# Performance work log

Measured on AMD Instinct MI355X. Metric: run time of the kernel, lower is better.

## Reference

```python
import jax, jax.numpy as jnp
import numpy as np
import math

B, S, D, H, DH, R = 2, 2048, 1024, 16, 64, 8
EPS = 1e-5


def setup_inputs() -> dict:
    key = jax.random.key(0)
    ks = jax.random.split(key, 8)
    hidden_states = jax.random.normal(ks[0], (B, S, D), jnp.float32)
    # causal boolean mask (batch, seq, seq); every row has >=1 valid entry
    causal = jnp.tril(jnp.ones((S, S), dtype=bool))
    attention_mask = jnp.broadcast_to(causal, (B, S, S))
    # lora: (n_layers=1, 4, batch, hidden, rank); [0]=qA,[1]=kA,[2]=qB,[3]=kB
    lora = jax.random.normal(ks[1], (1, 4, B, D, R), jnp.float32) * 0.02
    ln_w = jnp.ones((D,), jnp.float32)
    Wq = jax.random.normal(ks[2], (D, D), jnp.float32) * 0.02
    Wk = jax.random.normal(ks[3], (D, D), jnp.float32) * 0.02
    Wv = jax.random.normal(ks[4], (D, D), jnp.float32) * 0.02
    Wo = jax.random.normal(ks[5], (D, D), jnp.float32) * 0.02
    return dict(hidden_states=hidden_states, attention_mask=attention_mask,
                lora=lora, ln_w=ln_w, Wq=Wq, Wk=Wk, Wv=Wv, Wo=Wo)


def _rms_ln(x, w):
    # model_center LayerNorm with bias=False == RMS layernorm
    var = jnp.mean(x * x, axis=-1, keepdims=True)
    return x * jax.lax.rsqrt(var + EPS) * w


def _lora_delta(h, A, Bm):
    # h: (b,s,D), A: (b,D,R), Bm: (b,R,D);  h + (h@A)@Bm * 2
    z = jnp.einsum('bsd,bdr->bsr', h, A)
    return h + jnp.einsum('bsr,brd->bsd', z, Bm) * 2


def reference(hidden_states, attention_mask, lora, ln_w, Wq, Wk, Wv, Wo):
    b, s, _ = hidden_states.shape
    x = _rms_ln(hidden_states, ln_w)
    h_q = x @ Wq.T
    h_k = x @ Wk.T
    h_v = x @ Wv.T
    layer = lora[0]  # (4, b, D, R)
    h_q = _lora_delta(h_q, layer[0], jnp.swapaxes(layer[2], 1, 2))
    h_k = _lora_delta(h_k, layer[1], jnp.swapaxes(layer[3], 1, 2))
    q = h_q.reshape(b, s, H, DH)
    k = h_k.reshape(b, s, H, DH)
    v = h_v.reshape(b, s, H, DH)
    score = jnp.einsum('bqhd,bkhd->bhqk', q, k) / math.sqrt(DH)
    m = attention_mask[:, None, :, :]  # (b,1,s,s)
    score = jnp.where(m, score, -jnp.inf)
    p = jax.nn.softmax(score, axis=-1)
    p = jnp.where(m, p, jnp.float32(0))
    out = jnp.einsum('bhqk,bkhd->bqhd', p, v).reshape(b, s, H * DH)
    out = out @ Wo.T
    return hidden_states + out
```

## Files before the change

### kernel.cpp

```cpp
#include <hip/hip_runtime.h>

typedef __bf16 bf16;
typedef __bf16 bf16x4 __attribute__((ext_vector_type(4)));
typedef __bf16 bf16x8 __attribute__((ext_vector_type(8)));
typedef float f32x4 __attribute__((ext_vector_type(4)));

#define DM 1024
#define NROW 4096
#define SEQ 2048
#define HDIM 64
#define NEGBIG -30000.0f

#define SWB(base, row, bcol) \
  ((char*)(base) + (row) * 128 + ((bcol) ^ (((row) & 7) << 4)))

__device__ __forceinline__ void async16(const bf16* g, bf16* l) {
  __builtin_amdgcn_global_load_lds(
      (const __attribute__((address_space(1))) unsigned int*)g,
      (__attribute__((address_space(3))) unsigned int*)l, 16, 0, 0);
}

template <bool F32OUT>
__device__ __forceinline__ void gemm128(const bf16* __restrict__ A,
                                        const bf16* __restrict__ Bw,
                                        bf16* __restrict__ Cb,
                                        float* __restrict__ Cf,
                                        const float* __restrict__ resid,
                                        int m0, int n0) {
  __shared__ __align__(16) bf16 sA[128 * 32];
  __shared__ __align__(16) bf16 sB[128 * 32];
  const int t = threadIdx.x;
  const int lane = t & 63;
  const int w = t >> 6;
  const int wm = (w & 1) * 64;
  const int wn = (w >> 1) * 64;
  const int lr = lane & 15;
  const int kg = lane >> 4;

  f32x4 acc[4][4];
#pragma unroll
  for (int i = 0; i < 4; i++)
#pragma unroll
    for (int j = 0; j < 4; j++)
#pragma unroll
      for (int r = 0; r < 4; r++) acc[i][j][r] = 0.0f;

  const int srow = t >> 2;
  const int scol = (t & 3) * 8;
  const bf16* gA = A + (size_t)(m0 + srow) * DM + scol;
  const bf16* gB = Bw + (size_t)(n0 + srow) * DM + scol;
  bf16* lA = &sA[t * 8];
  bf16* lB = &sB[t * 8];

  for (int k0 = 0; k0 < DM; k0 += 32) {
    async16(gA + k0, lA);
    async16(gA + k0 + 64 * DM, lA + 2048);
    async16(gB + k0, lB);
    async16(gB + k0 + 64 * DM, lB + 2048);
    __syncthreads();
    bf16x8 av[4], bv[4];
#pragma unroll
    for (int mi = 0; mi < 4; mi++)
      av[mi] = *(const bf16x8*)&sA[(wm + mi * 16 + lr) * 32 + kg * 8];
#pragma unroll
    for (int nj = 0; nj < 4; nj++)
      bv[nj] = *(const bf16x8*)&sB[(wn + nj * 16 + lr) * 32 + kg * 8];
#pragma unroll
    for (int mi = 0; mi < 4; mi++)
#pragma unroll
      for (int nj = 0; nj < 4; nj++)
        acc[mi][nj] = __builtin_amdgcn_mfma_f32_16x16x32_bf16(av[mi], bv[nj],
                                                              acc[mi][nj], 0, 0, 0);
    __syncthreads();
  }

#pragma unroll
  for (int mi = 0; mi < 4; mi++) {
#pragma unroll
    for (int r = 0; r < 4; r++) {
      const int grow = m0 + wm + mi * 16 + kg * 4 + r;
      const size_t base = (size_t)grow * DM + n0 + wn + lr;
#pragma unroll
      for (int nj = 0; nj < 4; nj++) {
        float v = acc[mi][nj][r];
        if (F32OUT) {
          Cf[base + nj * 16] = v + resid[base + nj * 16];
        } else {
          Cb[base + nj * 16] = (bf16)v;
        }
      }
    }
  }
}

__global__ __launch_bounds__(256) void k_pre(const float* __restrict__ hin,
                                             const float* __restrict__ wln,
                                             const float* __restrict__ Wq,
                                             const float* __restrict__ Wk,
                                             const float* __restrict__ Wv,
                                             const float* __restrict__ Wo,
                                             bf16* __restrict__ xo,
                                             bf16* __restrict__ wcast) {
  __shared__ float red[4];
  const int t = threadIdx.x;
  const int bb = blockIdx.x;
  if (bb < NROW) {
    const int row = bb;
    const float4 h4 = ((const float4*)(hin + (size_t)row * DM))[t];
    float ss = h4.x * h4.x + h4.y * h4.y + h4.z * h4.z + h4.w * h4.w;
#pragma unroll
    for (int off = 1; off < 64; off <<= 1) ss += __shfl_xor(ss, off, 64);
    if ((t & 63) == 0) red[t >> 6] = ss;
    __syncthreads();
    ss = red[0] + red[1] + red[2] + red[3];
    const float inv = rsqrtf(ss * (1.0f / DM) + 1e-5f);
    const float4 w4 = ((const float4*)wln)[t];
    bf16x4 o;
    o[0] = (bf16)(h4.x * inv * w4.x);
    o[1] = (bf16)(h4.y * inv * w4.y);
    o[2] = (bf16)(h4.z * inv * w4.z);
    o[3] = (bf16)(h4.w * inv * w4.w);
    *(bf16x4*)&xo[(size_t)row * DM + t * 4] = o;
  } else {
    const int i = (bb - NROW) * 256 + t;
    const int mat = i >> 18;
    const int off = i & 262143;
    const float* s = (mat == 0) ? Wq : (mat == 1) ? Wk : (mat == 2) ? Wv : Wo;
    const float4 v = ((const float4*)s)[off];
    bf16x4 o;
    o[0] = (bf16)v.x; o[1] = (bf16)v.y; o[2] = (bf16)v.z; o[3] = (bf16)v.w;
    ((bf16x4*)wcast)[i] = o;
  }
}

__global__ __launch_bounds__(256) void k_qkv(const bf16* __restrict__ x,
                                             const bf16* __restrict__ Wq,
                                             const bf16* __restrict__ Wk,
                                             const bf16* __restrict__ Wv,
                                             bf16* __restrict__ hq,
                                             bf16* __restrict__ hk,
                                             bf16* __restrict__ hv) {
  const int nb = blockIdx.y;
  const int wsel = nb >> 3;
  const int n0 = (nb & 7) * 128;
  const bf16* Bw = (wsel == 0) ? Wq : (wsel == 1) ? Wk : Wv;
  bf16* C = (wsel == 0) ? hq : (wsel == 1) ? hk : hv;
  gemm128<false>(x, Bw, C, nullptr, nullptr, blockIdx.x * 128, n0);
}

__global__ __launch_bounds__(256) void k_oproj(const bf16* __restrict__ ctx,
                                               const bf16* __restrict__ Wo,
                                               const float* __restrict__ resid,
                                               float* __restrict__ out) {
  gemm128<true>(ctx, Wo, nullptr, out, resid, blockIdx.x * 128, blockIdx.y * 128);
}

__global__ __launch_bounds__(256) void k_mid(const bf16* __restrict__ hv,
                                             bf16* __restrict__ hvT,
                                             bf16* __restrict__ hq,
                                             bf16* __restrict__ hk,
                                             const float* __restrict__ lora) {
  __shared__ __align__(16) char smem[18432];
  const int t = threadIdx.x;
  const int bb = blockIdx.x;
  const int lane = t & 63;
  const int w = t >> 6;
  const int lr = lane & 15;
  const int kg = lane >> 4;

  if (bb < 1024) {
    bf16* sT = (bf16*)smem;
    const int s0 = (bb & 31) * 64;
    const int c0 = ((bb >> 5) & 15) * 64;
    const int b = bb >> 9;
    const int r = t >> 2;
    const int cc = (t & 3) * 16;
    const bf16* g = hv + ((size_t)(b * SEQ + s0 + r)) * DM + c0 + cc;
    const bf16x8 a0 = *(const bf16x8*)g;
    const bf16x8 a1 = *(const bf16x8*)(g + 8);
    *(bf16x8*)SWB(sT, r, cc * 2) = a0;
    *(bf16x8*)SWB(sT, r, cc * 2 + 16) = a1;
    __syncthreads();
    bf16x8 o0, o1;
#pragma unroll
    for (int j = 0; j < 8; j++) {
      o0[j] = *(const bf16*)SWB(sT, cc + j, r * 2);
      o1[j] = *(const bf16*)SWB(sT, cc + 8 + j, r * 2);
    }
    bf16* o = hvT + ((size_t)(b * DM + c0 + r)) * SEQ + s0 + cc;
    *(bf16x8*)o = o0;
    *(bf16x8*)(o + 8) = o1;
  } else {
    bf16* At = (bf16*)smem;
    float* Zp = (float*)(smem + 16384);
    const int lid = bb - 1024;
    const int row0 = (lid & 127) * 32;
    const int which = lid >> 7;
    const int b = row0 >> 11;
    bf16* H = (which == 0 ? hq : hk) + (size_t)row0 * DM;
    const float* Am = lora + (size_t)(which == 0 ? 0 : 1) * 16384 + (size_t)b * 8192;
    const float* Bm = lora + (size_t)(which == 0 ? 2 : 3) * 16384 + (size_t)b * 8192;

    const int d0 = lane * 16;
    float4 Bv[32];
    {
      const float4* bp = (const float4*)(Bm + (size_t)d0 * 8);
#pragma unroll
      for (int i = 0; i < 32; i++) Bv[i] = bp[i];
    }

    {
      const float4* ap = (const float4*)(Am + (size_t)t * 32);
#pragma unroll
      for (int i = 0; i < 8; i++) {
        const float4 v = ap[i];
        const int idx = t * 32 + i * 4;
        At[(idx & 7) * 1024 + (idx >> 3)]             = (bf16)v.x;
        At[((idx + 1) & 7) * 1024 + ((idx + 1) >> 3)] = (bf16)v.y;
        At[((idx + 2) & 7) * 1024 + ((idx + 2) >> 3)] = (bf16)v.z;
        At[((idx + 3) & 7) * 1024 + ((idx + 3) >> 3)] = (bf16)v.w;
      }
    }
    __syncthreads();

    const int tile = w & 1;
    const int khalf = w >> 1;
    {
      f32x4 zacc;
#pragma unroll
      for (int r = 0; r < 4; r++) zacc[r] = 0.f;
      const bf16* gH = H + (size_t)(tile * 16 + lr) * DM + khalf * 512 + kg * 8;
      const bf16* lA = &At[(lr & 7) * 1024 + khalf * 512 + kg * 8];
#pragma unroll
      for (int i = 0; i < 16; i++) {
        const bf16x8 ah = *(const bf16x8*)(gH + i * 32);
        const bf16x8 ba = *(const bf16x8*)(lA + i * 32);
        zacc = __builtin_amdgcn_mfma_f32_16x16x32_bf16(ah, ba, zacc, 0, 0, 0);
      }
      if (lr < 8) {
#pragma unroll
        for (int r = 0; r < 4; r++)
          Zp[(khalf * 32 + tile * 16 + kg * 4 + r) * 8 + lr] = zacc[r];
      }
    }
    __syncthreads();

#pragma unroll
    for (int rr = 0; rr < 8; rr++) {
      const int row = w * 8 + rr;
      const float4 z0 = *(const float4*)&Zp[(row) * 8 + 0];
      const float4 z1 = *(const float4*)&Zp[(row) * 8 + 4];
      const float4 y0 = *(const float4*)&Zp[(32 + row) * 8 + 0];
      const float4 y1 = *(const float4*)&Zp[(32 + row) * 8 + 4];
      const float za = z0.x + y0.x, zb = z0.y + y0.y, zc = z0.z + y0.z, zd = z0.w + y0.w;
      const float ze = z1.x + y1.x, zf = z1.y + y1.y, zg = z1.z + y1.z, zh = z1.w + y1.w;
      bf16* hp = H + (size_t)row * DM + d0;
      const bf16x8 h0 = *(const bf16x8*)hp;
      const bf16x8 h1 = *(const bf16x8*)(hp + 8);
      bf16x8 o0, o1;
#pragma unroll
      for (int j = 0; j < 16; j++) {
        const float4 b0 = Bv[2 * j];
        const float4 b1 = Bv[2 * j + 1];
        const float delta = za * b0.x + zb * b0.y + zc * b0.z + zd * b0.w +
                            ze * b1.x + zf * b1.y + zg * b1.z + zh * b1.w;
        const float hj = (j < 8) ? (float)h0[j] : (float)h1[j - 8];
        const bf16 ov = (bf16)(hj + 2.0f * delta);
        if (j < 8) o0[j] = ov; else o1[j - 8] = ov;
      }
      *(bf16x8*)hp = o0;
      *(bf16x8*)(hp + 8) = o1;
    }
  }
}

__global__ __launch_bounds__(256, 3) void k_attn(const bf16* __restrict__ hq,
                                                 const bf16* __restrict__ hk,
                                                 const bf16* __restrict__ hvT,
                                                 bf16* __restrict__ ctx) {
  const int n = blockIdx.x;
  const int slab = n & 31;
  const int hh = slab & 15;
  const int b = slab >> 4;
  const int xx = n >> 5;
  const int s = xx >> 3;
  const int v = xx & 7;
  const int qt = (s == 0) ? 4 * v : (s == 1) ? 31 - 4 * v
               : (s == 2) ? 4 * v + 2 : 29 - 4 * v;
  const int qbase = qt * 64;

  const int t = threadIdx.x;
  const int lane = t & 63;
  const int w = t >> 6;
  const int lr = lane & 15;
  const int kg = lane >> 4;

  __shared__ __align__(16) bf16 sQ[64 * 64];
  __shared__ __align__(16) bf16 sK[2][64 * 64];
  __shared__ __align__(16) bf16 sVt[2][64 * 64];
  __shared__ __align__(16) bf16 sP[64 * 64];

  const size_t rowbase = (size_t)b * SEQ;
  const int hoff = hh * HDIM;
  const float sscale = 0.18033688011112042f;

  {
    const int r4 = t >> 2;
    const int ce = (t & 3) * 16;
    const int cb = (t & 3) * 32;
    const bf16* g = hq + (rowbase + qbase + r4) * DM + hoff + ce;
    bf16x8 q0 = *(const bf16x8*)g;
    bf16x8 q1 = *(const bf16x8*)(g + 8);
    bf16x8 o0, o1;
#pragma unroll
    for (int j = 0; j < 8; j++) {
      o0[j] = (bf16)((float)q0[j] * sscale);
      o1[j] = (bf16)((float)q1[j] * sscale);
    }
    *(bf16x8*)SWB(sQ, r4, cb) = o0;
    *(bf16x8*)SWB(sQ, r4, cb + 16) = o1;
  }

  const int l3 = lane >> 3;
  const int dcol = ((lane & 7) ^ l3) * 8;
  const int drow = w * 16 + l3;
  const bf16* gKb = hk + (rowbase + drow) * DM + hoff + dcol;
  const bf16* gVb = hvT + ((size_t)slab * HDIM + drow) * SEQ + dcol;
  bf16* lK = &sK[0][0] + w * 1024 + lane * 8;
  bf16* lV = &sVt[0][0] + w * 1024 + lane * 8;

#define ISSUE_KV(kt_, buf_)                                          \
  {                                                                  \
    const bf16* gk_ = gKb + (size_t)(kt_) * 64 * DM;                 \
    const bf16* gv_ = gVb + (kt_) * 64;                              \
    bf16* lk_ = lK + (buf_) * 4096;                                  \
    bf16* lv_ = lV + (buf_) * 4096;                                  \
    async16(gk_, lk_);                                               \
    async16(gk_ + 8 * DM, lk_ + 512);                                \
    async16(gv_, lv_);                                               \
    async16(gv_ + 8 * SEQ, lv_ + 512);                               \
  }

  ISSUE_KV(0, 0);

  float m_l = NEGBIG, l_l = 0.f;
  f32x4 oacc[4];
#pragma unroll
  for (int nj = 0; nj < 4; nj++)
#pragma unroll
    for (int r = 0; r < 4; r++) oacc[nj][r] = 0.f;

  asm volatile("s_waitcnt vmcnt(0)" ::: "memory");
  __syncthreads();

  for (int kt = 0; kt <= qt; kt++) {
    const int cur = kt & 1;
    if (kt < qt) ISSUE_KV(kt + 1, cur ^ 1);
    const bf16* sKc = &sK[cur][0];
    const bf16* sVc = &sVt[cur][0];

    f32x4 sc[4];
#pragma unroll
    for (int nj = 0; nj < 4; nj++)
#pragma unroll
      for (int r = 0; r < 4; r++) sc[nj][r] = 0.f;
    __builtin_amdgcn_s_setprio(1);
#pragma unroll
    for (int ks = 0; ks < 2; ks++) {
      const bf16x8 bq = *(const bf16x8*)SWB(sQ, w * 16 + lr, ks * 64 + kg * 16);
#pragma unroll
      for (int nj = 0; nj < 4; nj++) {
        const bf16x8 ak = *(const bf16x8*)SWB(sKc, nj * 16 + lr, ks * 64 + kg * 16);
        sc[nj] = __builtin_amdgcn_mfma_f32_16x16x32_bf16(ak, bq, sc[nj], 0, 0, 0);
      }
    }
    __builtin_amdgcn_s_setprio(0);

    if (kt == qt) {
      const int ql = w * 16 + lr;
#pragma unroll
      for (int nj = 0; nj < 4; nj++)
#pragma unroll
        for (int r = 0; r < 4; r++) {
          const int kl = nj * 16 + kg * 4 + r;
          sc[nj][r] = (kl <= ql) ? sc[nj][r] : NEGBIG;
        }
    }

    float rm = sc[0][0];
#pragma unroll
    for (int nj = 0; nj < 4; nj++)
#pragma unroll
      for (int r = 0; r < 4; r++) rm = fmaxf(rm, sc[nj][r]);
    rm = fmaxf(rm, __shfl_xor(rm, 16, 64));
    rm = fmaxf(rm, __shfl_xor(rm, 32, 64));
    const float mnew = fmaxf(m_l, rm);
    const float alpha = __builtin_amdgcn_exp2f(m_l - mnew);
    float rs = 0.f;
#pragma unroll
    for (int nj = 0; nj < 4; nj++)
#pragma unroll
      for (int r = 0; r < 4; r++) {
        const float p = __builtin_amdgcn_exp2f(sc[nj][r] - mnew);
        sc[nj][r] = p;
        rs += p;
      }
    rs += __shfl_xor(rs, 16, 64);
    rs += __shfl_xor(rs, 32, 64);
    l_l = l_l * alpha + rs;
    m_l = mnew;

#pragma unroll
    for (int nj = 0; nj < 4; nj++) {
      bf16x4 p4;
#pragma unroll
      for (int r = 0; r < 4; r++) p4[r] = (bf16)sc[nj][r];
      *(bf16x4*)SWB(sP, w * 16 + lr, nj * 32 + kg * 8) = p4;
    }

#pragma unroll
    for (int r = 0; r < 4; r++) {
      const float ar = __shfl(alpha, (lane & 48) | (kg * 4 + r), 64);
#pragma unroll
      for (int nj = 0; nj < 4; nj++) oacc[nj][r] *= ar;
    }

    __builtin_amdgcn_s_setprio(1);
#pragma unroll
    for (int ks = 0; ks < 2; ks++) {
      const bf16x8 ap = *(const bf16x8*)SWB(sP, w * 16 + lr, ks * 64 + kg * 16);
#pragma unroll
      for (int nj = 0; nj < 4; nj++) {
        const bf16x8 bv = *(const bf16x8*)SWB(sVc, nj * 16 + lr, ks * 64 + kg * 16);
        oacc[nj] = __builtin_amdgcn_mfma_f32_16x16x32_bf16(ap, bv, oacc[nj], 0, 0, 0);
      }
    }
    __builtin_amdgcn_s_setprio(0);

    asm volatile("s_waitcnt vmcnt(0)" ::: "memory");
    __syncthreads();
  }

#pragma unroll
  for (int r = 0; r < 4; r++) {
    const float lrow = __shfl(l_l, (lane & 48) | (kg * 4 + r), 64);
    const float invl = 1.0f / lrow;
    const int qr = qbase + w * 16 + kg * 4 + r;
    const size_t base = (rowbase + qr) * DM + hoff + lr;
#pragma unroll
    for (int nj = 0; nj < 4; nj++)
      ctx[base + nj * 16] = (bf16)(oacc[nj][r] * invl);
  }
}

extern "C" void kernel_launch(void* const* d_in, const int* in_sizes, int n_in,
                              void* d_out, int out_size, void* d_ws, size_t ws_size,
                              hipStream_t stream) {
  const float* hidden = (const float*)d_in[0];
  const float* lora = (const float*)d_in[2];
  const float* wln  = (const float*)d_in[3];
  const float* Wq   = (const float*)d_in[4];
  const float* Wk   = (const float*)d_in[5];
  const float* Wv   = (const float*)d_in[6];
  const float* Wo   = (const float*)d_in[7];
  float* out = (float*)d_out;

  const size_t BUF = (size_t)NROW * DM;
  if (ws_size < 4 * BUF * sizeof(bf16)) return;
  bf16* ws = (bf16*)d_ws;
  bf16* hq  = ws;
  bf16* hk  = ws + 1 * BUF;
  bf16* hv  = ws + 2 * BUF;
  bf16* ctx = ws + 3 * BUF;

  bf16* dob = (bf16*)d_out;
  bf16* x   = dob;
  bf16* wqb = dob + BUF;
  bf16* wkb = dob + BUF + DM * DM;
  bf16* wvb = dob + BUF + 2 * DM * DM;
  bf16* wob = dob + BUF + 3 * DM * DM;
  bf16* hvT = dob;

  k_pre<<<dim3(2 * NROW), dim3(256), 0, stream>>>(hidden, wln, Wq, Wk, Wv, Wo, x, wqb);
  k_qkv<<<dim3(32, 24), dim3(256), 0, stream>>>(x, wqb, wkb, wvb, hq, hk, hv);
  k_mid<<<dim3(1280), dim3(256), 0, stream>>>(hv, hvT, hq, hk, lora);
  k_attn<<<dim3(1024), dim3(256), 0, stream>>>(hq, hk, hvT, ctx);
  k_oproj<<<dim3(32, 8), dim3(256), 0, stream>>>(ctx, wob, hidden, out);
}
```

Baseline: 226.8 us.

## Double-buffer GEMM LDS tiles and switch attention KV to register prefetch

The GEMM main loop now double-buffers its A/B LDS tiles, issuing the next k-slice's async global-to-LDS loads before the current MFMAs, and raises wave priority around the MFMA block. The attention kernel drops its double-buffered async K/V LDS staging. Instead it prefetches the next K/V tile into registers and writes them into single LDS buffers each iteration, which cuts LDS use and allows launch bounds to go from 3 to 4 blocks per SM. The GEMM change targets load latency. The attention change trades async copies for register staging to gain occupancy, at the cost of extra VGPRs and explicit LDS stores.

Result: faster. 219.2 us (-3.3%).

```diff
diff --git a/kernel.cpp b/kernel.cpp
--- a/kernel.cpp
+++ b/kernel.cpp
@@ -27,8 +27,8 @@
                                         float* __restrict__ Cf,
                                         const float* __restrict__ resid,
                                         int m0, int n0) {
-  __shared__ __align__(16) bf16 sA[128 * 32];
-  __shared__ __align__(16) bf16 sB[128 * 32];
+  __shared__ __align__(16) bf16 sA[2][128 * 32];
+  __shared__ __align__(16) bf16 sB[2][128 * 32];
   const int t = threadIdx.x;
   const int lane = t & 63;
   const int w = t >> 6;
@@ -49,30 +49,39 @@
   const int scol = (t & 3) * 8;
   const bf16* gA = A + (size_t)(m0 + srow) * DM + scol;
   const bf16* gB = Bw + (size_t)(n0 + srow) * DM + scol;
-  bf16* lA = &sA[t * 8];
-  bf16* lB = &sB[t * 8];
+
+#define GSTAGE(k0_, buf_)                                \
+  {                                                      \
+    async16(gA + (k0_), &sA[buf_][t * 8]);               \
+    async16(gA + (k0_) + 64 * DM, &sA[buf_][t * 8 + 2048]); \
+    async16(gB + (k0_), &sB[buf_][t * 8]);               \
+    async16(gB + (k0_) + 64 * DM, &sB[buf_][t * 8 + 2048]); \
+  }
+
+  GSTAGE(0, 0);
+  __syncthreads();
 
   for (int k0 = 0; k0 < DM; k0 += 32) {
-    async16(gA + k0, lA);
-    async16(gA + k0 + 64 * DM, lA + 2048);
-    async16(gB + k0, lB);
-    async16(gB + k0 + 64 * DM, lB + 2048);
-    __syncthreads();
+    const int cur = (k0 >> 5) & 1;
+    if (k0 + 32 < DM) GSTAGE(k0 + 32, cur ^ 1);
     bf16x8 av[4], bv[4];
 #pragma unroll
     for (int mi = 0; mi < 4; mi++)
-      av[mi] = *(const bf16x8*)&sA[(wm + mi * 16 + lr) * 32 + kg * 8];
+      av[mi] = *(const bf16x8*)&sA[cur][(wm + mi * 16 + lr) * 32 + kg * 8];
 #pragma unroll
     for (int nj = 0; nj < 4; nj++)
-      bv[nj] = *(const bf16x8*)&sB[(wn + nj * 16 + lr) * 32 + kg * 8];
+      bv[nj] = *(const bf16x8*)&sB[cur][(wn + nj * 16 + lr) * 32 + kg * 8];
+    __builtin_amdgcn_s_setprio(1);
 #pragma unroll
     for (int mi = 0; mi < 4; mi++)
 #pragma unroll
       for (int nj = 0; nj < 4; nj++)
         acc[mi][nj] = __builtin_amdgcn_mfma_f32_16x16x32_bf16(av[mi], bv[nj],
                                                               acc[mi][nj], 0, 0, 0);
-    __syncthreads();
-  }
+    __builtin_amdgcn_s_setprio(0);
+    __syncthreads();
+  }
+#undef GSTAGE
 
 #pragma unroll
   for (int mi = 0; mi < 4; mi++) {
@@ -274,7 +283,7 @@
   }
 }
 
-__global__ __launch_bounds__(256, 3) void k_attn(const bf16* __restrict__ hq,
+__global__ __launch_bounds__(256, 4) void k_attn(const bf16* __restrict__ hq,
                                                  const bf16* __restrict__ hk,
                                                  const bf16* __restrict__ hvT,
                                                  bf16* __restrict__ ctx) {
@@ -296,18 +305,19 @@
   const int kg = lane >> 4;
 
   __shared__ __align__(16) bf16 sQ[64 * 64];
-  __shared__ __align__(16) bf16 sK[2][64 * 64];
-  __shared__ __align__(16) bf16 sVt[2][64 * 64];
+  __shared__ __align__(16) bf16 sK[64 * 64];
+  __shared__ __align__(16) bf16 sVt[64 * 64];
   __shared__ __align__(16) bf16 sP[64 * 64];
 
   const size_t rowbase = (size_t)b * SEQ;
   const int hoff = hh * HDIM;
   const float sscale = 0.18033688011112042f;
 
+  const int r4 = t >> 2;
+  const int ce = (t & 3) * 16;
+  const int cb = (t & 3) * 32;
+
   {
-    const int r4 = t >> 2;
-    const int ce = (t & 3) * 16;
-    const int cb = (t & 3) * 32;
     const bf16* g = hq + (rowbase + qbase + r4) * DM + hoff + ce;
     bf16x8 q0 = *(const bf16x8*)g;
     bf16x8 q1 = *(const bf16x8*)(g + 8);
@@ -321,27 +331,12 @@
     *(bf16x8*)SWB(sQ, r4, cb + 16) = o1;
   }
 
-  const int l3 = lane >> 3;
-  const int dcol = ((lane & 7) ^ l3) * 8;
-  const int drow = w * 16 + l3;
-  const bf16* gKb = hk + (rowbase + drow) * DM + hoff + dcol;
-  const bf16* gVb = hvT + ((size_t)slab * HDIM + drow) * SEQ + dcol;
-  bf16* lK = &sK[0][0] + w * 1024 + lane * 8;
-  bf16* lV = &sVt[0][0] + w * 1024 + lane * 8;
-
-#define ISSUE_KV(kt_, buf_)                                          \
-  {                                                                  \
-    const bf16* gk_ = gKb + (size_t)(kt_) * 64 * DM;                 \
-    const bf16* gv_ = gVb + (kt_) * 64;                              \
-    bf16* lk_ = lK + (buf_) * 4096;                                  \
-    bf16* lv_ = lV + (buf_) * 4096;                                  \
-    async16(gk_, lk_);                                               \
-    async16(gk_ + 8 * DM, lk_ + 512);                                \
-    async16(gv_, lv_);                                               \
-    async16(gv_ + 8 * SEQ, lv_ + 512);                               \
-  }
-
-  ISSUE_KV(0, 0);
+  const bf16* gK = hk + (rowbase + r4) * DM + hoff + ce;
+  const bf16* gV = hvT + ((size_t)slab * HDIM + r4) * SEQ + ce;
+  bf16x8 kr0 = *(const bf16x8*)gK;
+  bf16x8 kr1 = *(const bf16x8*)(gK + 8);
+  bf16x8 vr0 = *(const bf16x8*)gV;
+  bf16x8 vr1 = *(const bf16x8*)(gV + 8);
 
   float m_l = NEGBIG, l_l = 0.f;
   f32x4 oacc[4];
@@ -350,14 +345,23 @@
 #pragma unroll
     for (int r = 0; r < 4; r++) oacc[nj][r] = 0.f;
 
-  asm volatile("s_waitcnt vmcnt(0)" ::: "memory");
   __syncthreads();
 
   for (int kt = 0; kt <= qt; kt++) {
-    const int cur = kt & 1;
-    if (kt < qt) ISSUE_KV(kt + 1, cur ^ 1);
-    const bf16* sKc = &sK[cur][0];
-    const bf16* sVc = &sVt[cur][0];
+    *(bf16x8*)SWB(sK, r4, cb) = kr0;
+    *(bf16x8*)SWB(sK, r4, cb + 16) = kr1;
+    *(bf16x8*)SWB(sVt, r4, cb) = vr0;
+    *(bf16x8*)SWB(sVt, r4, cb + 16) = vr1;
+    __syncthreads();
+
+    if (kt < qt) {
+      const bf16* gK2 = gK + (size_t)(kt + 1) * 64 * DM;
+      const bf16* gV2 = gV + (kt + 1) * 64;
+      kr0 = *(const bf16x8*)gK2;
+      kr1 = *(const bf16x8*)(gK2 + 8);
+      vr0 = *(const bf16x8*)gV2;
+      vr1 = *(const bf16x8*)(gV2 + 8);
+    }
 
     f32x4 sc[4];
 #pragma unroll
@@ -370,7 +374,7 @@
       const bf16x8 bq = *(const bf16x8*)SWB(sQ, w * 16 + lr, ks * 64 + kg * 16);
 #pragma unroll
       for (int nj = 0; nj < 4; nj++) {
-        const bf16x8 ak = *(const bf16x8*)SWB(sKc, nj * 16 + lr, ks * 64 + kg * 16);
+        const bf16x8 ak = *(const bf16x8*)SWB(sK, nj * 16 + lr, ks * 64 + kg * 16);
         sc[nj] = __builtin_amdgcn_mfma_f32_16x16x32_bf16(ak, bq, sc[nj], 0, 0, 0);
       }
     }
@@ -431,13 +435,11 @@
       const bf16x8 ap = *(const bf16x8*)SWB(sP, w * 16 + lr, ks * 64 + kg * 16);
 #pragma unroll
       for (int nj = 0; nj < 4; nj++) {
-        const bf16x8 bv = *(const bf16x8*)SWB(sVc, nj * 16 + lr, ks * 64 + kg * 16);
+        const bf16x8 bv = *(const bf16x8*)SWB(sVt, nj * 16 + lr, ks * 64 + kg * 16);
         oacc[nj] = __builtin_amdgcn_mfma_f32_16x16x32_bf16(ap, bv, oacc[nj], 0, 0, 0);
       }
     }
     __builtin_amdgcn_s_setprio(0);
-
-    asm volatile("s_waitcnt vmcnt(0)" ::: "memory");
     __syncthreads();
   }
 
```
